# Optimization experiments

Measured on AMD Instinct MI355X. Metric: run time of the kernel, lower is better.

Reference implementation:

```python
import jax, jax.numpy as jnp
import numpy as np

N = 4096   # support size
B = 512    # number of histograms (columns)


def setup_inputs() -> dict:
    key = jax.random.key(0)
    kU, kP, kK = jax.random.split(key, 3)
    # u must satisfy u < lamda; uniform [0,1) with lamda=10 is safe.
    U = jax.random.uniform(kU, (N, B), dtype=jnp.float32)
    # strictly positive histograms (avoid log(0))
    P = jax.random.uniform(kP, (N, B), dtype=jnp.float32) + 0.01
    # positive Gibbs kernel
    K = jax.random.uniform(kK, (N, N), dtype=jnp.float32) + 1e-3
    return {"U": U, "P": P, "K": K, "eps": 1, "lamda": 10}


def reference(U, P, K, eps, lamda):
    """Vectorized OTModel.OT_unbal: sum over columns of the primal unbalanced OT
    value reconstructed from dual potential U.  gamma_ij = a_i * K_ij * f_j is
    never materialized; all reductions over gamma are contracted analytically.
    """
    eps = jnp.float32(eps)
    lamda = jnp.float32(lamda)
    # f in log domain: (lamda/eps) * log(lamda/(lamda-u))          [N, B]
    flog = (lamda / eps) * jnp.log(lamda / (lamda - U))
    f = jnp.exp(flog)
    # alpha/eps with the mean-scale stabilization from get_alpha_unbal
    scale = flog.mean(axis=0)                                      # [B]
    KF_stab = K @ jnp.exp(flog - scale)                            # [N, B]
    alpha_over_eps = jnp.log(P) - (jnp.log(KF_stab) + scale)       # [N, B]
    a = jnp.exp(alpha_over_eps)                                    # exp(alpha/eps)
    Kf = K @ f                                                     # [N, B]
    # (gamma @ flog).sum() = sum_i a_i * (K @ (f * flog))_i
    term1 = jnp.sum(a * (K @ (f * flog)))
    # (gamma.T @ (alpha/eps)).sum() = sum_i a_i * (alpha/eps)_i * (K @ f)_i
    term2 = jnp.sum(a * alpha_over_eps * Kf)
    # gamma.sum()
    term3 = jnp.sum(a * Kf)
    # gamma.sum(0)_j = f_j * (K^T @ a)_j
    gcol = f * (K.T @ a)                                           # [N, B]
    # q from get_q_unbal (unstabilized, as in the original)
    q = (lamda / (lamda - U)) ** (lamda / eps + 1.0) * (K.T @ (P / Kf))
    # KL(a,b) = sum(a*log(a/b) - a)   (inputs strictly positive here)
    kl = jnp.sum(gcol * jnp.log(gcol / q) - gcol)
    return eps * (term1 + term2 - term3) + lamda * kl
```

## Files before the change

### kernel.cpp

```cpp
#include <hip/hip_runtime.h>

#define NN 4096
#define BB 512

typedef __attribute__((ext_vector_type(4))) float f32x4;
typedef unsigned short ushort;
typedef unsigned char uchar;
typedef unsigned int uint;

#define ASCALE 16384.0f
#define AINV   6.103515625e-05f

__device__ __forceinline__ float scal_val(const void* p) {
    int b = *(const int*)p;
    if (b >= 1 && b <= 1000000) return (float)b;
    return __int_as_float(b);
}

__device__ __forceinline__ uint pack4_fp8(float a, float b, float c, float d) {
    int v = __builtin_amdgcn_cvt_pk_fp8_f32(a, b, 0, false);
    v = __builtin_amdgcn_cvt_pk_fp8_f32(c, d, v, true);
    return (uint)v;
}

__device__ __forceinline__ void gload16(const void* g, void* l) {
    __builtin_amdgcn_global_load_lds(
        (const __attribute__((address_space(1))) unsigned int*)g,
        (__attribute__((address_space(3))) unsigned int*)l, 16, 0, 0);
}

__device__ __forceinline__ double wave_sum(double v) {
#pragma unroll
    for (int s = 32; s > 0; s >>= 1) v += __shfl_down(v, s, 64);
    return v;
}



__global__ __launch_bounds__(256) void k_prep(const float* __restrict__ K,
                                              const float* __restrict__ U,
                                              uchar* __restrict__ Kb,
                                              uchar* __restrict__ KTb,
                                              uchar* __restrict__ fT,
                                              uchar* __restrict__ gT,
                                              const void* epsp, const void* lamp) {
    __shared__ float tile[64][65];
    __shared__ float tg[64][65];
    const int t = threadIdx.x;
    const int tx = t & 15, ty = t >> 4;
    const int bid = blockIdx.x;

    if (bid < 4096) {
        const int c0 = (bid & 63) * 64, r0 = (bid >> 6) * 64;
#pragma unroll
        for (int it = 0; it < 4; ++it) {
            int row = ty + it * 16;
            float4 v = *(const float4*)&K[(size_t)(r0 + row) * NN + c0 + tx * 4];
            *(uint*)&Kb[(size_t)(r0 + row) * NN + c0 + tx * 4] =
                pack4_fp8(v.x, v.y, v.z, v.w);
            tile[row][tx * 4 + 0] = v.x;
            tile[row][tx * 4 + 1] = v.y;
            tile[row][tx * 4 + 2] = v.z;
            tile[row][tx * 4 + 3] = v.w;
        }
        __syncthreads();
#pragma unroll
        for (int it = 0; it < 4; ++it) {
            int row = ty + it * 16;
            *(uint*)&KTb[(size_t)(c0 + row) * NN + r0 + tx * 4] =
                pack4_fp8(tile[tx * 4 + 0][row], tile[tx * 4 + 1][row],
                          tile[tx * 4 + 2][row], tile[tx * 4 + 3][row]);
        }
    } else {
        const int r = bid - 4096;
        const int c0 = (r & 7) * 64;
        const int r0 = (r >> 3) * 64;
        const float eps = scal_val(epsp), lam = scal_val(lamp);
        const float rr = lam / eps;
#pragma unroll
        for (int it = 0; it < 4; ++it) {
            int row = ty + it * 16;
            float4 v = *(const float4*)&U[(size_t)(r0 + row) * BB + c0 + tx * 4];
            float uu[4] = {v.x, v.y, v.z, v.w};
#pragma unroll
            for (int k = 0; k < 4; ++k) {
                float L = __logf(lam / (lam - uu[k]));
                float fl = rr * L;
                float fv = __expf(fl);
                tile[row][tx * 4 + k] = fv;
                tg[row][tx * 4 + k] = fv * fl;
            }
        }
        __syncthreads();
#pragma unroll
        for (int it = 0; it < 4; ++it) {
            int row = ty + it * 16;
            *(uint*)&fT[(size_t)(c0 + row) * NN + r0 + tx * 4] =
                pack4_fp8(tile[tx * 4 + 0][row], tile[tx * 4 + 1][row],
                          tile[tx * 4 + 2][row], tile[tx * 4 + 3][row]);
            *(uint*)&gT[(size_t)(c0 + row) * NN + r0 + tx * 4] =
                pack4_fp8(tg[tx * 4 + 0][row], tg[tx * 4 + 1][row],
                          tg[tx * 4 + 2][row], tg[tx * 4 + 3][row]);
        }
    }
}

__global__ __launch_bounds__(256) void k_gemm1(const uchar* __restrict__ Kb,
                                               const uchar* __restrict__ fT,
                                               const uchar* __restrict__ gT,
                                               float* __restrict__ Y1p,
                                               float* __restrict__ Y2p) {
    __shared__ __align__(16) uchar As[2][128 * 64];
    __shared__ __align__(16) uchar Bf[2][64 * 64];
    __shared__ __align__(16) uchar Bg[2][64 * 64];

    const int tid = threadIdx.x;
    const int lane = tid & 63;
    const int w = tid >> 6;
    const int wm = w & 1, wn = w >> 1;
    const int bid = blockIdx.x;
    const int kh = bid & 1;
    const int i0 = ((bid >> 1) & 31) * 128;
    const int j0 = (bid >> 6) * 64;
    const int quad = lane >> 4;
    const int l15 = lane & 15;
    const int sw = (l15 >> 1) & 3;

    f32x4 zero = {0.f, 0.f, 0.f, 0.f};
    f32x4 accf[4][2], accg[4][2];
#pragma unroll
    for (int mt = 0; mt < 4; ++mt)
#pragma unroll
        for (int nt = 0; nt < 2; ++nt) { accf[mt][nt] = zero; accg[mt][nt] = zero; }

    const int rl = lane >> 2;
    const int goff = ((lane & 3) ^ ((rl >> 1) & 3)) * 16;

    auto stage = [&](int k0, int b) {
#pragma unroll
        for (int it = 0; it < 2; ++it) {
            const int rbase = w * 32 + it * 16;
            gload16(Kb + (size_t)(i0 + rbase + rl) * NN + k0 + goff,
                    &As[b][rbase * 64]);
        }
        const int rbase = w * 16;
        gload16(fT + (size_t)(j0 + rbase + rl) * NN + k0 + goff, &Bf[b][rbase * 64]);
        gload16(gT + (size_t)(j0 + rbase + rl) * NN + k0 + goff, &Bg[b][rbase * 64]);
    };

    const int kbase = kh * (NN / 2);
    stage(kbase, 0);
    __syncthreads();
    for (int step = 0; step < NN / 128; ++step) {
        const int cur = step & 1;
        if (step < NN / 128 - 1) stage(kbase + (step + 1) * 64, cur ^ 1);
#pragma unroll
        for (int ks = 0; ks < 2; ++ks) {
            const int c = ks * 4 + quad;
            const int co = (((c >> 1) ^ sw) << 4) | ((c & 1) << 3);
            long af[4];
#pragma unroll
            for (int mt = 0; mt < 4; ++mt)
                af[mt] = *(const long*)&As[cur][(wm * 64 + mt * 16 + l15) * 64 + co];
            long bfv[2], bgv[2];
#pragma unroll
            for (int nt = 0; nt < 2; ++nt) {
                bfv[nt] = *(const long*)&Bf[cur][(wn * 32 + nt * 16 + l15) * 64 + co];
                bgv[nt] = *(const long*)&Bg[cur][(wn * 32 + nt * 16 + l15) * 64 + co];
            }
#pragma unroll
            for (int mt = 0; mt < 4; ++mt)
#pragma unroll
                for (int nt = 0; nt < 2; ++nt) {
                    accf[mt][nt] = __builtin_amdgcn_mfma_f32_16x16x32_fp8_fp8(
                        af[mt], bfv[nt], accf[mt][nt], 0, 0, 0);
                    accg[mt][nt] = __builtin_amdgcn_mfma_f32_16x16x32_fp8_fp8(
                        af[mt], bgv[nt], accg[mt][nt], 0, 0, 0);
                }
        }
        __syncthreads();
    }

    float* o1 = Y1p + (size_t)kh * NN * BB;
    float* o2 = Y2p + (size_t)kh * NN * BB;
#pragma unroll
    for (int mt = 0; mt < 4; ++mt)
#pragma unroll
        for (int nt = 0; nt < 2; ++nt) {
            const int ib = i0 + wm * 64 + mt * 16 + quad * 4;
            const int j = j0 + wn * 32 + nt * 16 + l15;
#pragma unroll
            for (int r = 0; r < 4; ++r) {
                o1[(size_t)(ib + r) * BB + j] = accf[mt][nt][r];
                o2[(size_t)(ib + r) * BB + j] = accg[mt][nt][r];
            }
        }
}

__global__ __launch_bounds__(256) void k_epi(const float* __restrict__ Y1p,
                                             const float* __restrict__ Y2p,
                                             const float* __restrict__ P,
                                             uchar* __restrict__ aT,
                                             double* __restrict__ parts) {
    __shared__ float ta[64][65];
    __shared__ double bred[4][3];
    const int t = threadIdx.x;
    const int lane = t & 63;
    const int w = t >> 6;
    const int tx = t & 15, ty = t >> 4;
    const int j0 = blockIdx.x * 64;
    const int i0 = blockIdx.y * 64;
    const int bid = blockIdx.y * 8 + blockIdx.x;
    const size_t H = (size_t)NN * BB;

    double t1 = 0.0, t2 = 0.0, t3 = 0.0;
#pragma unroll
    for (int it = 0; it < 4; ++it) {
        int row = ty + it * 16;
        size_t off = (size_t)(i0 + row) * BB + j0 + tx * 4;
        float4 a1 = *(const float4*)(Y1p + off);
        float4 b1 = *(const float4*)(Y1p + H + off);
        float4 a2 = *(const float4*)(Y2p + off);
        float4 b2 = *(const float4*)(Y2p + H + off);
        float4 p4 = *(const float4*)(P + off);
        float y1[4] = {a1.x + b1.x, a1.y + b1.y, a1.z + b1.z, a1.w + b1.w};
        float y2[4] = {a2.x + b2.x, a2.y + b2.y, a2.z + b2.z, a2.w + b2.w};
        float pv[4] = {p4.x, p4.y, p4.z, p4.w};
#pragma unroll
        for (int e = 0; e < 4; ++e) {
            float aij = pv[e] / y1[e];
            t1 += (double)(aij * y2[e]);
            t2 += (double)(pv[e] * __logf(aij));
            t3 += (double)pv[e];
            ta[row][tx * 4 + e] = aij * ASCALE;
        }
    }
    __syncthreads();
#pragma unroll
    for (int it = 0; it < 4; ++it) {
        int row = ty + it * 16;
        *(uint*)&aT[(size_t)(j0 + row) * NN + i0 + tx * 4] =
            pack4_fp8(ta[tx * 4 + 0][row], ta[tx * 4 + 1][row],
                      ta[tx * 4 + 2][row], ta[tx * 4 + 3][row]);
    }

    t1 = wave_sum(t1); t2 = wave_sum(t2); t3 = wave_sum(t3);
    if (lane == 0) { bred[w][0] = t1; bred[w][1] = t2; bred[w][2] = t3; }
    __syncthreads();
    if (t == 0) {
        double a = 0, b = 0, c = 0;
#pragma unroll
        for (int ww = 0; ww < 4; ++ww) { a += bred[ww][0]; b += bred[ww][1]; c += bred[ww][2]; }
        parts[bid] = a;
        parts[512 + bid] = b;
        parts[1024 + bid] = c;
    }
}

__global__ __launch_bounds__(256) void k_gemm2(const uchar* __restrict__ KTb,
                                               const uchar* __restrict__ aT,
                                               const float* __restrict__ U,
                                               const void* epsp, const void* lamp,
                                               double* __restrict__ parts) {
    __shared__ __align__(16) uchar As[2][128 * 64];
    __shared__ __align__(16) uchar Bs[2][64 * 64];
    __shared__ double bred[4];

    const float eps = scal_val(epsp), lam = scal_val(lamp);
    const float rr = lam / eps;
    const int tid = threadIdx.x;
    const int lane = tid & 63;
    const int w = tid >> 6;
    const int wm = w & 1, wn = w >> 1;
    const int bid = blockIdx.x;
    const int kh = bid & 1;
    const int i0 = ((bid >> 1) & 31) * 128;
    const int j0 = (bid >> 6) * 64;
    const int quad = lane >> 4;
    const int l15 = lane & 15;
    const int sw = (l15 >> 1) & 3;

    f32x4 zero = {0.f, 0.f, 0.f, 0.f};
    f32x4 accs[4][2];
#pragma unroll
    for (int mt = 0; mt < 4; ++mt)
#pragma unroll
        for (int nt = 0; nt < 2; ++nt) accs[mt][nt] = zero;

    const int rl = lane >> 2;
    const int goff = ((lane & 3) ^ ((rl >> 1) & 3)) * 16;

    auto stage = [&](int k0, int b) {
#pragma unroll
        for (int it = 0; it < 2; ++it) {
            const int rbase = w * 32 + it * 16;
            gload16(KTb + (size_t)(i0 + rbase + rl) * NN + k0 + goff,
                    &As[b][rbase * 64]);
        }
        const int rbase = w * 16;
        gload16(aT + (size_t)(j0 + rbase + rl) * NN + k0 + goff, &Bs[b][rbase * 64]);
    };

    const int kbase = kh * (NN / 2);
    stage(kbase, 0);
    __syncthreads();
    for (int step = 0; step < NN / 128; ++step) {
        const int cur = step & 1;
        if (step < NN / 128 - 1) stage(kbase + (step + 1) * 64, cur ^ 1);
#pragma unroll
        for (int ks = 0; ks < 2; ++ks) {
            const int c = ks * 4 + quad;
            const int co = (((c >> 1) ^ sw) << 4) | ((c & 1) << 3);
            long af[4];
#pragma unroll
            for (int mt = 0; mt < 4; ++mt)
                af[mt] = *(const long*)&As[cur][(wm * 64 + mt * 16 + l15) * 64 + co];
            long bv[2];
#pragma unroll
            for (int nt = 0; nt < 2; ++nt)
                bv[nt] = *(const long*)&Bs[cur][(wn * 32 + nt * 16 + l15) * 64 + co];
#pragma unroll
            for (int mt = 0; mt < 4; ++mt)
#pragma unroll
                for (int nt = 0; nt < 2; ++nt)
                    accs[mt][nt] = __builtin_amdgcn_mfma_f32_16x16x32_fp8_fp8(
                        af[mt], bv[nt], accs[mt][nt], 0, 0, 0);
        }
        __syncthreads();
    }

    double klp = 0.0;
#pragma unroll
    for (int mt = 0; mt < 4; ++mt)
#pragma unroll
        for (int nt = 0; nt < 2; ++nt) {
            const int ib = i0 + wm * 64 + mt * 16 + quad * 4;
            const int j = j0 + wn * 32 + nt * 16 + l15;
#pragma unroll
            for (int r = 0; r < 4; ++r) {
                float s = accs[mt][nt][r] * AINV;
                float u = U[(size_t)(ib + r) * BB + j];
                float L = __logf(lam / (lam - u));
                float fv = __expf(rr * L);
                klp -= (double)(fv * (1.0f + L) * s);
            }
        }

    klp = wave_sum(klp);
    if (lane == 0) bred[w] = klp;
    __syncthreads();
    if (tid == 0) parts[1536 + bid] = bred[0] + bred[1] + bred[2] + bred[3];
}

__global__ __launch_bounds__(256) void k_final(const double* __restrict__ parts,
                                               const void* epsp, const void* lamp,
                                               float* __restrict__ out) {
    __shared__ double red[4][4];
    const int tid = threadIdx.x;
    const int lane = tid & 63, w = tid >> 6;
    double s0 = 0.0, s1 = 0.0, s2 = 0.0, s3 = 0.0;
    for (int i = tid; i < 512; i += 256) {
        s0 += parts[i];
        s1 += parts[512 + i];
        s2 += parts[1024 + i];
        s3 += parts[1536 + i];
    }
    s0 = wave_sum(s0); s1 = wave_sum(s1); s2 = wave_sum(s2); s3 = wave_sum(s3);
    if (lane == 0) { red[w][0] = s0; red[w][1] = s1; red[w][2] = s2; red[w][3] = s3; }
    __syncthreads();
    if (tid == 0) {
        double t1 = 0, t2 = 0, t3 = 0, kl = 0;
#pragma unroll
        for (int ww = 0; ww < 4; ++ww) {
            t1 += red[ww][0]; t2 += red[ww][1]; t3 += red[ww][2]; kl += red[ww][3];
        }
        float eps = scal_val(epsp), lam = scal_val(lamp);
        out[0] = (float)((double)eps * (t1 + t2 - t3) + (double)lam * kl);
    }
}

extern "C" void kernel_launch(void* const* d_in, const int* in_sizes, int n_in,
                              void* d_out, int out_size, void* d_ws, size_t ws_size,
                              hipStream_t stream) {
    const float* U = (const float*)d_in[0];
    const float* P = (const float*)d_in[1];
    const float* K = (const float*)d_in[2];
    const void* epsp = d_in[3];
    const void* lamp = d_in[4];

    double* parts = (double*)d_ws;
    char* base = (char*)d_ws + (64 << 10);
    uchar* Kb  = (uchar*)base;
    uchar* KTb = (uchar*)(base + ((size_t)16 << 20));
    uchar* fT  = (uchar*)(base + ((size_t)32 << 20));
    uchar* gT  = (uchar*)(base + ((size_t)34 << 20));
    uchar* aT  = (uchar*)(base + ((size_t)36 << 20));
    float* Y1p = (float*)(base + ((size_t)38 << 20));
    float* Y2p = (float*)(base + ((size_t)54 << 20));

    k_prep<<<4608, 256, 0, stream>>>(K, U, Kb, KTb, fT, gT, epsp, lamp);
    k_gemm1<<<512, 256, 0, stream>>>(Kb, fT, gT, Y1p, Y2p);
    k_epi<<<dim3(8, 64), 256, 0, stream>>>(Y1p, Y2p, P, aT, parts);
    k_gemm2<<<512, 256, 0, stream>>>(KTb, aT, U, epsp, lamp, parts);
    k_final<<<1, 256, 0, stream>>>(parts, epsp, lamp, (float*)d_out);
}
```

Before: 191.9 us.

## Move term1 into second GEMM epilogue, drop g GEMM, split-K by four

Term1 is re-expressed as sum over K^T a times f*flog, so it is computed in the second GEMM's epilogue and the f*flog operand and its GEMM disappear from the first GEMM. Both GEMMs switch to 4-way split-K with 1024 blocks. The fp8 K dimension is permuted in global memory so each lane reads 16 contiguous bytes per LDS load for two MFMAs. This removes half the work of the first GEMM and the Y2 round trip, at the cost of an extra partial-sum buffer that the epilogue kernel must read.

New measurement: 171.2 us. 10.8% less time.

```diff
diff --git a/kernel.cpp b/kernel.cpp
--- a/kernel.cpp
+++ b/kernel.cpp
@@ -4,6 +4,7 @@
 #define BB 512
 
 typedef __attribute__((ext_vector_type(4))) float f32x4;
+typedef __attribute__((ext_vector_type(2))) long long2v;
 typedef unsigned short ushort;
 typedef unsigned char uchar;
 typedef unsigned int uint;
@@ -35,6 +36,10 @@
     return v;
 }
 
+__device__ __forceinline__ int kperm(int kk) {
+    int c = kk >> 3;
+    return (c & 3) * 16 + (c >> 2) * 8 + (kk & 7);
+}
 
 
 __global__ __launch_bounds__(256) void k_prep(const float* __restrict__ K,
@@ -42,13 +47,12 @@
                                               uchar* __restrict__ Kb,
                                               uchar* __restrict__ KTb,
                                               uchar* __restrict__ fT,
-                                              uchar* __restrict__ gT,
                                               const void* epsp, const void* lamp) {
     __shared__ float tile[64][65];
-    __shared__ float tg[64][65];
     const int t = threadIdx.x;
     const int tx = t & 15, ty = t >> 4;
     const int bid = blockIdx.x;
+    const int pp = kperm(tx * 4);
 
     if (bid < 4096) {
         const int c0 = (bid & 63) * 64, r0 = (bid >> 6) * 64;
@@ -56,7 +60,7 @@
         for (int it = 0; it < 4; ++it) {
             int row = ty + it * 16;
             float4 v = *(const float4*)&K[(size_t)(r0 + row) * NN + c0 + tx * 4];
-            *(uint*)&Kb[(size_t)(r0 + row) * NN + c0 + tx * 4] =
+            *(uint*)&Kb[(size_t)(r0 + row) * NN + c0 + pp] =
                 pack4_fp8(v.x, v.y, v.z, v.w);
             tile[row][tx * 4 + 0] = v.x;
             tile[row][tx * 4 + 1] = v.y;
@@ -67,7 +71,7 @@
 #pragma unroll
         for (int it = 0; it < 4; ++it) {
             int row = ty + it * 16;
-            *(uint*)&KTb[(size_t)(c0 + row) * NN + r0 + tx * 4] =
+            *(uint*)&KTb[(size_t)(c0 + row) * NN + r0 + pp] =
                 pack4_fp8(tile[tx * 4 + 0][row], tile[tx * 4 + 1][row],
                           tile[tx * 4 + 2][row], tile[tx * 4 + 3][row]);
         }
@@ -85,56 +89,47 @@
 #pragma unroll
             for (int k = 0; k < 4; ++k) {
                 float L = __logf(lam / (lam - uu[k]));
-                float fl = rr * L;
-                float fv = __expf(fl);
-                tile[row][tx * 4 + k] = fv;
-                tg[row][tx * 4 + k] = fv * fl;
+                tile[row][tx * 4 + k] = __expf(rr * L);
             }
         }
         __syncthreads();
 #pragma unroll
         for (int it = 0; it < 4; ++it) {
             int row = ty + it * 16;
-            *(uint*)&fT[(size_t)(c0 + row) * NN + r0 + tx * 4] =
+            *(uint*)&fT[(size_t)(c0 + row) * NN + r0 + pp] =
                 pack4_fp8(tile[tx * 4 + 0][row], tile[tx * 4 + 1][row],
                           tile[tx * 4 + 2][row], tile[tx * 4 + 3][row]);
-            *(uint*)&gT[(size_t)(c0 + row) * NN + r0 + tx * 4] =
-                pack4_fp8(tg[tx * 4 + 0][row], tg[tx * 4 + 1][row],
-                          tg[tx * 4 + 2][row], tg[tx * 4 + 3][row]);
         }
     }
 }
 
 __global__ __launch_bounds__(256) void k_gemm1(const uchar* __restrict__ Kb,
                                                const uchar* __restrict__ fT,
-                                               const uchar* __restrict__ gT,
-                                               float* __restrict__ Y1p,
-                                               float* __restrict__ Y2p) {
+                                               float* __restrict__ Y1p) {
     __shared__ __align__(16) uchar As[2][128 * 64];
     __shared__ __align__(16) uchar Bf[2][64 * 64];
-    __shared__ __align__(16) uchar Bg[2][64 * 64];
 
     const int tid = threadIdx.x;
     const int lane = tid & 63;
     const int w = tid >> 6;
     const int wm = w & 1, wn = w >> 1;
     const int bid = blockIdx.x;
-    const int kh = bid & 1;
-    const int i0 = ((bid >> 1) & 31) * 128;
-    const int j0 = (bid >> 6) * 64;
+    const int kh = bid & 3;
+    const int i0 = ((bid >> 2) & 31) * 128;
+    const int j0 = (bid >> 7) * 64;
     const int quad = lane >> 4;
     const int l15 = lane & 15;
     const int sw = (l15 >> 1) & 3;
 
     f32x4 zero = {0.f, 0.f, 0.f, 0.f};
-    f32x4 accf[4][2], accg[4][2];
+    f32x4 acc[4][2];
 #pragma unroll
     for (int mt = 0; mt < 4; ++mt)
 #pragma unroll
-        for (int nt = 0; nt < 2; ++nt) { accf[mt][nt] = zero; accg[mt][nt] = zero; }
+        for (int nt = 0; nt < 2; ++nt) acc[mt][nt] = zero;
 
     const int rl = lane >> 2;
-    const int goff = ((lane & 3) ^ ((rl >> 1) & 3)) * 16;
+    const int goff = ((lane & 3) ^ ((lane >> 3) & 3)) * 16;
 
     auto stage = [&](int k0, int b) {
 #pragma unroll
@@ -143,46 +138,37 @@
             gload16(Kb + (size_t)(i0 + rbase + rl) * NN + k0 + goff,
                     &As[b][rbase * 64]);
         }
-        const int rbase = w * 16;
-        gload16(fT + (size_t)(j0 + rbase + rl) * NN + k0 + goff, &Bf[b][rbase * 64]);
-        gload16(gT + (size_t)(j0 + rbase + rl) * NN + k0 + goff, &Bg[b][rbase * 64]);
+        gload16(fT + (size_t)(j0 + w * 16 + rl) * NN + k0 + goff,
+                &Bf[b][(w * 16) * 64]);
     };
 
-    const int kbase = kh * (NN / 2);
+    const int kbase = kh * (NN / 4);
     stage(kbase, 0);
     __syncthreads();
-    for (int step = 0; step < NN / 128; ++step) {
+    const int uoff = ((quad ^ sw) << 4);
+    for (int step = 0; step < NN / 256; ++step) {
         const int cur = step & 1;
-        if (step < NN / 128 - 1) stage(kbase + (step + 1) * 64, cur ^ 1);
-#pragma unroll
-        for (int ks = 0; ks < 2; ++ks) {
-            const int c = ks * 4 + quad;
-            const int co = (((c >> 1) ^ sw) << 4) | ((c & 1) << 3);
-            long af[4];
-#pragma unroll
-            for (int mt = 0; mt < 4; ++mt)
-                af[mt] = *(const long*)&As[cur][(wm * 64 + mt * 16 + l15) * 64 + co];
-            long bfv[2], bgv[2];
+        if (step < NN / 256 - 1) stage(kbase + (step + 1) * 64, cur ^ 1);
+        long2v av[4], bv[2];
+#pragma unroll
+        for (int mt = 0; mt < 4; ++mt)
+            av[mt] = *(const long2v*)&As[cur][(wm * 64 + mt * 16 + l15) * 64 + uoff];
+#pragma unroll
+        for (int nt = 0; nt < 2; ++nt)
+            bv[nt] = *(const long2v*)&Bf[cur][(wn * 32 + nt * 16 + l15) * 64 + uoff];
+#pragma unroll
+        for (int mt = 0; mt < 4; ++mt)
 #pragma unroll
             for (int nt = 0; nt < 2; ++nt) {
-                bfv[nt] = *(const long*)&Bf[cur][(wn * 32 + nt * 16 + l15) * 64 + co];
-                bgv[nt] = *(const long*)&Bg[cur][(wn * 32 + nt * 16 + l15) * 64 + co];
+                acc[mt][nt] = __builtin_amdgcn_mfma_f32_16x16x32_fp8_fp8(
+                    av[mt].x, bv[nt].x, acc[mt][nt], 0, 0, 0);
+                acc[mt][nt] = __builtin_amdgcn_mfma_f32_16x16x32_fp8_fp8(
+                    av[mt].y, bv[nt].y, acc[mt][nt], 0, 0, 0);
             }
-#pragma unroll
-            for (int mt = 0; mt < 4; ++mt)
-#pragma unroll
-                for (int nt = 0; nt < 2; ++nt) {
-                    accf[mt][nt] = __builtin_amdgcn_mfma_f32_16x16x32_fp8_fp8(
-                        af[mt], bfv[nt], accf[mt][nt], 0, 0, 0);
-                    accg[mt][nt] = __builtin_amdgcn_mfma_f32_16x16x32_fp8_fp8(
-                        af[mt], bgv[nt], accg[mt][nt], 0, 0, 0);
-                }
-        }
         __syncthreads();
     }
 
     float* o1 = Y1p + (size_t)kh * NN * BB;
-    float* o2 = Y2p + (size_t)kh * NN * BB;
 #pragma unroll
     for (int mt = 0; mt < 4; ++mt)
 #pragma unroll
@@ -190,20 +176,17 @@
             const int ib = i0 + wm * 64 + mt * 16 + quad * 4;
             const int j = j0 + wn * 32 + nt * 16 + l15;
 #pragma unroll
-            for (int r = 0; r < 4; ++r) {
-                o1[(size_t)(ib + r) * BB + j] = accf[mt][nt][r];
-                o2[(size_t)(ib + r) * BB + j] = accg[mt][nt][r];
-            }
+            for (int r = 0; r < 4; ++r)
+                o1[(size_t)(ib + r) * BB + j] = acc[mt][nt][r];
         }
 }
 
 __global__ __launch_bounds__(256) void k_epi(const float* __restrict__ Y1p,
-                                             const float* __restrict__ Y2p,
                                              const float* __restrict__ P,
                                              uchar* __restrict__ aT,
                                              double* __restrict__ parts) {
     __shared__ float ta[64][65];
-    __shared__ double bred[4][3];
+    __shared__ double bred[4][2];
     const int t = threadIdx.x;
     const int lane = t & 63;
     const int w = t >> 6;
@@ -212,24 +195,24 @@
     const int i0 = blockIdx.y * 64;
     const int bid = blockIdx.y * 8 + blockIdx.x;
     const size_t H = (size_t)NN * BB;
-
-    double t1 = 0.0, t2 = 0.0, t3 = 0.0;
+    const int pp = kperm(tx * 4);
+
+    double t2 = 0.0, t3 = 0.0;
 #pragma unroll
     for (int it = 0; it < 4; ++it) {
         int row = ty + it * 16;
         size_t off = (size_t)(i0 + row) * BB + j0 + tx * 4;
         float4 a1 = *(const float4*)(Y1p + off);
         float4 b1 = *(const float4*)(Y1p + H + off);
-        float4 a2 = *(const float4*)(Y2p + off);
-        float4 b2 = *(const float4*)(Y2p + H + off);
+        float4 c1 = *(const float4*)(Y1p + 2 * H + off);
+        float4 d1 = *(const float4*)(Y1p + 3 * H + off);
         float4 p4 = *(const float4*)(P + off);
-        float y1[4] = {a1.x + b1.x, a1.y + b1.y, a1.z + b1.z, a1.w + b1.w};
-        float y2[4] = {a2.x + b2.x, a2.y + b2.y, a2.z + b2.z, a2.w + b2.w};
+        float y1[4] = {a1.x + b1.x + c1.x + d1.x, a1.y + b1.y + c1.y + d1.y,
+                       a1.z + b1.z + c1.z + d1.z, a1.w + b1.w + c1.w + d1.w};
         float pv[4] = {p4.x, p4.y, p4.z, p4.w};
 #pragma unroll
         for (int e = 0; e < 4; ++e) {
             float aij = pv[e] / y1[e];
-            t1 += (double)(aij * y2[e]);
             t2 += (double)(pv[e] * __logf(aij));
             t3 += (double)pv[e];
             ta[row][tx * 4 + e] = aij * ASCALE;
@@ -239,21 +222,20 @@
 #pragma unroll
     for (int it = 0; it < 4; ++it) {
         int row = ty + it * 16;
-        *(uint*)&aT[(size_t)(j0 + row) * NN + i0 + tx * 4] =
+        *(uint*)&aT[(size_t)(j0 + row) * NN + i0 + pp] =
             pack4_fp8(ta[tx * 4 + 0][row], ta[tx * 4 + 1][row],
                       ta[tx * 4 + 2][row], ta[tx * 4 + 3][row]);
     }
 
-    t1 = wave_sum(t1); t2 = wave_sum(t2); t3 = wave_sum(t3);
-    if (lane == 0) { bred[w][0] = t1; bred[w][1] = t2; bred[w][2] = t3; }
+    t2 = wave_sum(t2); t3 = wave_sum(t3);
+    if (lane == 0) { bred[w][0] = t2; bred[w][1] = t3; }
     __syncthreads();
     if (t == 0) {
-        double a = 0, b = 0, c = 0;
-#pragma unroll
-        for (int ww = 0; ww < 4; ++ww) { a += bred[ww][0]; b += bred[ww][1]; c += bred[ww][2]; }
-        parts[bid] = a;
-        parts[512 + bid] = b;
-        parts[1024 + bid] = c;
+        double b = 0, c = 0;
+#pragma unroll
+        for (int ww = 0; ww < 4; ++ww) { b += bred[ww][0]; c += bred[ww][1]; }
+        parts[2048 + bid] = b;
+        parts[2560 + bid] = c;
     }
 }
 
@@ -264,7 +246,7 @@
                                                double* __restrict__ parts) {
     __shared__ __align__(16) uchar As[2][128 * 64];
     __shared__ __align__(16) uchar Bs[2][64 * 64];
-    __shared__ double bred[4];
+    __shared__ double bred[4][2];
 
     const float eps = scal_val(epsp), lam = scal_val(lamp);
     const float rr = lam / eps;
@@ -273,22 +255,22 @@
     const int w = tid >> 6;
     const int wm = w & 1, wn = w >> 1;
     const int bid = blockIdx.x;
-    const int kh = bid & 1;
-    const int i0 = ((bid >> 1) & 31) * 128;
-    const int j0 = (bid >> 6) * 64;
+    const int kh = bid & 3;
+    const int i0 = ((bid >> 2) & 31) * 128;
+    const int j0 = (bid >> 7) * 64;
     const int quad = lane >> 4;
     const int l15 = lane & 15;
     const int sw = (l15 >> 1) & 3;
 
     f32x4 zero = {0.f, 0.f, 0.f, 0.f};
-    f32x4 accs[4][2];
+    f32x4 acc[4][2];
 #pragma unroll
     for (int mt = 0; mt < 4; ++mt)
 #pragma unroll
-        for (int nt = 0; nt < 2; ++nt) accs[mt][nt] = zero;
+        for (int nt = 0; nt < 2; ++nt) acc[mt][nt] = zero;
 
     const int rl = lane >> 2;
-    const int goff = ((lane & 3) ^ ((rl >> 1) & 3)) * 16;
+    const int goff = ((lane & 3) ^ ((lane >> 3) & 3)) * 16;
 
     auto stage = [&](int k0, int b) {
 #pragma unroll
@@ -297,39 +279,37 @@
             gload16(KTb + (size_t)(i0 + rbase + rl) * NN + k0 + goff,
                     &As[b][rbase * 64]);
         }
-        const int rbase = w * 16;
-        gload16(aT + (size_t)(j0 + rbase + rl) * NN + k0 + goff, &Bs[b][rbase * 64]);
+        gload16(aT + (size_t)(j0 + w * 16 + rl) * NN + k0 + goff,
+                &Bs[b][(w * 16) * 64]);
     };
 
-    const int kbase = kh * (NN / 2);
+    const int kbase = kh * (NN / 4);
     stage(kbase, 0);
     __syncthreads();
-    for (int step = 0; step < NN / 128; ++step) {
+    const int uoff = ((quad ^ sw) << 4);
+    for (int step = 0; step < NN / 256; ++step) {
         const int cur = step & 1;
-        if (step < NN / 128 - 1) stage(kbase + (step + 1) * 64, cur ^ 1);
-#pragma unroll
-        for (int ks = 0; ks < 2; ++ks) {
-            const int c = ks * 4 + quad;
-            const int co = (((c >> 1) ^ sw) << 4) | ((c & 1) << 3);
-            long af[4];
-#pragma unroll
-            for (int mt = 0; mt < 4; ++mt)
-                af[mt] = *(const long*)&As[cur][(wm * 64 + mt * 16 + l15) * 64 + co];
-            long bv[2];
-#pragma unroll
-            for (int nt = 0; nt < 2; ++nt)
-                bv[nt] = *(const long*)&Bs[cur][(wn * 32 + nt * 16 + l15) * 64 + co];
-#pragma unroll
-            for (int mt = 0; mt < 4; ++mt)
-#pragma unroll
-                for (int nt = 0; nt < 2; ++nt)
-                    accs[mt][nt] = __builtin_amdgcn_mfma_f32_16x16x32_fp8_fp8(
-                        af[mt], bv[nt], accs[mt][nt], 0, 0, 0);
-        }
+        if (step < NN / 256 - 1) stage(kbase + (step + 1) * 64, cur ^ 1);
+        long2v av[4], bv[2];
+#pragma unroll
+        for (int mt = 0; mt < 4; ++mt)
+            av[mt] = *(const long2v*)&As[cur][(wm * 64 + mt * 16 + l15) * 64 + uoff];
+#pragma unroll
+        for (int nt = 0; nt < 2; ++nt)
+            bv[nt] = *(const long2v*)&Bs[cur][(wn * 32 + nt * 16 + l15) * 64 + uoff];
+#pragma unroll
+        for (int mt = 0; mt < 4; ++mt)
+#pragma unroll
+            for (int nt = 0; nt < 2; ++nt) {
+                acc[mt][nt] = __builtin_amdgcn_mfma_f32_16x16x32_fp8_fp8(
+                    av[mt].x, bv[nt].x, acc[mt][nt], 0, 0, 0);
+                acc[mt][nt] = __builtin_amdgcn_mfma_f32_16x16x32_fp8_fp8(
+                    av[mt].y, bv[nt].y, acc[mt][nt], 0, 0, 0);
+            }
         __syncthreads();
     }
 
-    double klp = 0.0;
+    double t1p = 0.0, klp = 0.0;
 #pragma unroll
     for (int mt = 0; mt < 4; ++mt)
 #pragma unroll
@@ -338,18 +318,25 @@
             const int j = j0 + wn * 32 + nt * 16 + l15;
 #pragma unroll
             for (int r = 0; r < 4; ++r) {
-                float s = accs[mt][nt][r] * AINV;
+                float s = acc[mt][nt][r] * AINV;
                 float u = U[(size_t)(ib + r) * BB + j];
                 float L = __logf(lam / (lam - u));
                 float fv = __expf(rr * L);
+                t1p += (double)(fv * rr * L * s);
                 klp -= (double)(fv * (1.0f + L) * s);
             }
         }
 
-    klp = wave_sum(klp);
-    if (lane == 0) bred[w] = klp;
-    __syncthreads();
-    if (tid == 0) parts[1536 + bid] = bred[0] + bred[1] + bred[2] + bred[3];
+    t1p = wave_sum(t1p); klp = wave_sum(klp);
+    if (lane == 0) { bred[w][0] = t1p; bred[w][1] = klp; }
+    __syncthreads();
+    if (tid == 0) {
+        double a = 0, b = 0;
+#pragma unroll
+        for (int ww = 0; ww < 4; ++ww) { a += bred[ww][0]; b += bred[ww][1]; }
+        parts[bid] = a;
+        parts[1024 + bid] = b;
+    }
 }
 
 __global__ __launch_bounds__(256) void k_final(const double* __restrict__ parts,
@@ -359,20 +346,22 @@
     const int tid = threadIdx.x;
     const int lane = tid & 63, w = tid >> 6;
     double s0 = 0.0, s1 = 0.0, s2 = 0.0, s3 = 0.0;
+    for (int i = tid; i < 1024; i += 256) {
+        s0 += parts[i];
+        s1 += parts[1024 + i];
+    }
     for (int i = tid; i < 512; i += 256) {
-        s0 += parts[i];
-        s1 += parts[512 + i];
-        s2 += parts[1024 + i];
-        s3 += parts[1536 + i];
+        s2 += parts[2048 + i];
+        s3 += parts[2560 + i];
     }
     s0 = wave_sum(s0); s1 = wave_sum(s1); s2 = wave_sum(s2); s3 = wave_sum(s3);
     if (lane == 0) { red[w][0] = s0; red[w][1] = s1; red[w][2] = s2; red[w][3] = s3; }
     __syncthreads();
     if (tid == 0) {
-        double t1 = 0, t2 = 0, t3 = 0, kl = 0;
+        double t1 = 0, kl = 0, t2 = 0, t3 = 0;
 #pragma unroll
         for (int ww = 0; ww < 4; ++ww) {
-            t1 += red[ww][0]; t2 += red[ww][1]; t3 += red[ww][2]; kl += red[ww][3];
+            t1 += red[ww][0]; kl += red[ww][1]; t2 += red[ww][2]; t3 += red[ww][3];
         }
         float eps = scal_val(epsp), lam = scal_val(lamp);
         out[0] = (float)((double)eps * (t1 + t2 - t3) + (double)lam * kl);
@@ -393,14 +382,12 @@
     uchar* Kb  = (uchar*)base;
     uchar* KTb = (uchar*)(base + ((size_t)16 << 20));
     uchar* fT  = (uchar*)(base + ((size_t)32 << 20));
-    uchar* gT  = (uchar*)(base + ((size_t)34 << 20));
-    uchar* aT  = (uchar*)(base + ((size_t)36 << 20));
-    float* Y1p = (float*)(base + ((size_t)38 << 20));
-    float* Y2p = (float*)(base + ((size_t)54 << 20));
-
-    k_prep<<<4608, 256, 0, stream>>>(K, U, Kb, KTb, fT, gT, epsp, lamp);
-    k_gemm1<<<512, 256, 0, stream>>>(Kb, fT, gT, Y1p, Y2p);
-    k_epi<<<dim3(8, 64), 256, 0, stream>>>(Y1p, Y2p, P, aT, parts);
-    k_gemm2<<<512, 256, 0, stream>>>(KTb, aT, U, epsp, lamp, parts);
+    uchar* aT  = (uchar*)(base + ((size_t)34 << 20));
+    float* Y1p = (float*)(base + ((size_t)36 << 20));
+
+    k_prep<<<4608, 256, 0, stream>>>(K, U, Kb, KTb, fT, epsp, lamp);
+    k_gemm1<<<1024, 256, 0, stream>>>(Kb, fT, Y1p);
+    k_epi<<<dim3(8, 64), 256, 0, stream>>>(Y1p, P, aT, parts);
+    k_gemm2<<<1024, 256, 0, stream>>>(KTb, aT, U, epsp, lamp, parts);
     k_final<<<1, 256, 0, stream>>>(parts, epsp, lamp, (float*)d_out);
 }
```
